# Kernel tuning notes

Hardware: AMD Instinct MI355X
Metric: run time of the kernel (lower is better)

The kernel has to match this reference:

```python
import jax, jax.numpy as jnp
import numpy as np

DIM = 1024
HEADS = 16
HEAD_DIM = DIM // HEADS
EPS = 1e-5


def _layer_norm(z, g, b):
    m = jnp.mean(z, axis=-1, keepdims=True)
    v = jnp.var(z, axis=-1, keepdims=True)
    return (z - m) * jax.lax.rsqrt(v + EPS) * g + b


def setup_inputs() -> dict:
    key = jax.random.key(0)
    ks = jax.random.split(key, 8)
    B, T, S = 2, 2048, 2048
    x = jax.random.normal(ks[0], (B, T, DIM), dtype=jnp.float32)
    context = jax.random.normal(ks[1], (B, S, DIM), dtype=jnp.float32)
    w_qkv = jax.random.normal(ks[2], (DIM, 3 * DIM), dtype=jnp.float32) * 0.02
    b_qkv = jnp.zeros((3 * DIM,), dtype=jnp.float32)
    w_out = jax.random.normal(ks[3], (DIM, DIM), dtype=jnp.float32) * 0.02
    b_out = jnp.zeros((DIM,), dtype=jnp.float32)
    ln_g = jnp.ones((DIM,), dtype=jnp.float32)
    ln_b = jnp.zeros((DIM,), dtype=jnp.float32)
    return {"x": x, "context": context, "w_qkv": w_qkv, "b_qkv": b_qkv,
            "w_out": w_out, "b_out": b_out, "ln_g": ln_g, "ln_b": ln_b}


def reference(x, context, w_qkv, b_qkv, w_out, b_out, ln_g, ln_b):
    B, T, C = x.shape
    S = context.shape[1]
    scale = HEAD_DIM ** -0.5

    def split_heads(z):  # [B, L, C] -> [B, H, L, Dh]
        return z.reshape(z.shape[0], z.shape[1], HEADS, HEAD_DIM).transpose(0, 2, 1, 3)

    # self qkv
    qkv = _layer_norm(x, ln_g, ln_b) @ w_qkv + b_qkv  # [B, T, 3C]
    q = split_heads(qkv[..., :C])
    k = split_heads(qkv[..., C:2 * C])
    v = split_heads(qkv[..., 2 * C:])

    # context k, v from the shared qkv projection (K/V slices)
    ckv = _layer_norm(context, ln_g, ln_b) @ w_qkv + b_qkv  # [B, S, 3C]
    ck = split_heads(ckv[..., C:2 * C])
    cv = split_heads(ckv[..., 2 * C:])

    k = jnp.concatenate([k, ck], axis=2)  # [B, H, T+S, Dh]
    v = jnp.concatenate([v, cv], axis=2)

    attn = jax.nn.softmax(jnp.einsum('bhtd,bhsd->bhts', q, k) * scale, axis=-1)
    out = jnp.einsum('bhts,bhsd->bhtd', attn, v)  # [B, H, T, Dh]
    out = out.transpose(0, 2, 1, 3).reshape(B, T, C)
    return out @ w_out + b_out + x
```

## Files before the change

kernel.cpp:

```cpp
#include <hip/hip_runtime.h>
#include <stdint.h>

#define H 16
#define DH 64
#define T 2048
#define SS 2048
#define L 4096
#define DIM 1024
#define BB 2

typedef __bf16 bf16x8 __attribute__((ext_vector_type(8)));
typedef float f32x4 __attribute__((ext_vector_type(4)));
typedef float f32x16 __attribute__((ext_vector_type(16)));
typedef unsigned u32x4 __attribute__((ext_vector_type(4)));

__device__ __forceinline__ unsigned short f2bf(float f){
  unsigned u = __builtin_bit_cast(unsigned, f);
  u += 0x7fff + ((u >> 16) & 1);
  return (unsigned short)(u >> 16);
}

__device__ __forceinline__ unsigned cvt_pk_bf16(float lo, float hi){
  unsigned r;
  asm("v_cvt_pk_bf16_f32 %0, %1, %2" : "=v"(r) : "v"(lo), "v"(hi));
  return r;
}

__device__ __forceinline__ float fmax3(float a, float b, float c){
  float r;
  asm("v_max3_f32 %0, %1, %2, %3" : "=v"(r) : "v"(a), "v"(b), "v"(c));
  return r;
}

__device__ __forceinline__ void gload_lds16(const void* g, void* l){
  void* gnc = const_cast<void*>(g);
  __builtin_amdgcn_global_load_lds((__attribute__((address_space(1))) void*)gnc,
                                   (__attribute__((address_space(3))) void*)l, 16, 0, 0);
}

__global__ __launch_bounds__(256) void ln_kernel(const float* __restrict__ x, const float* __restrict__ ctx,
                          const float* __restrict__ g, const float* __restrict__ b,
                          unsigned short* __restrict__ out){
  int row = blockIdx.x;
  int tid = threadIdx.x;
  const float* src = (row < BB*T) ? (x + (size_t)row*DIM) : (ctx + (size_t)(row - BB*T)*DIM);
  float4 v = reinterpret_cast<const float4*>(src)[tid];
  float s  = v.x + v.y + v.z + v.w;
  float s2 = v.x*v.x + v.y*v.y + v.z*v.z + v.w*v.w;
  #pragma unroll
  for (int off = 32; off > 0; off >>= 1){
    s  += __shfl_down(s,  off, 64);
    s2 += __shfl_down(s2, off, 64);
  }
  __shared__ float red[8];
  if ((tid & 63) == 0){ red[(tid>>6)*2] = s; red[(tid>>6)*2+1] = s2; }
  __syncthreads();
  s  = red[0] + red[2] + red[4] + red[6];
  s2 = red[1] + red[3] + red[5] + red[7];
  float mean = s * (1.0f/DIM);
  float var  = s2 * (1.0f/DIM) - mean*mean;
  float rstd = rsqrtf(var + 1e-5f);
  float4 gg = reinterpret_cast<const float4*>(g)[tid];
  float4 bv = reinterpret_cast<const float4*>(b)[tid];
  ushort4 o;
  o.x = f2bf((v.x-mean)*rstd*gg.x + bv.x);
  o.y = f2bf((v.y-mean)*rstd*gg.y + bv.y);
  o.z = f2bf((v.z-mean)*rstd*gg.z + bv.z);
  o.w = f2bf((v.w-mean)*rstd*gg.w + bv.w);
  reinterpret_cast<ushort4*>(out + (size_t)row*DIM)[tid] = o;
}

__global__ __launch_bounds__(256) void transpose_f32_bf16(const float* __restrict__ in,
                          unsigned short* __restrict__ out, int R, int C){
  __shared__ float tile[32][33];
  int c0 = blockIdx.x*32, r0 = blockIdx.y*32;
  int tx = threadIdx.x & 31, ty = threadIdx.x >> 5;
  #pragma unroll
  for (int k = 0; k < 4; k++)
    tile[ty + k*8][tx] = in[(size_t)(r0 + ty + k*8)*C + c0 + tx];
  __syncthreads();
  #pragma unroll
  for (int k = 0; k < 4; k++)
    out[(size_t)(c0 + ty + k*8)*R + r0 + tx] = f2bf(tile[tx][ty + k*8]);
}

__global__ __launch_bounds__(256) void qkv_gemm(const unsigned short* __restrict__ A,
      const unsigned short* __restrict__ Bt, const float* __restrict__ bias,
      unsigned short* __restrict__ qbuf, unsigned short* __restrict__ kbuf,
      unsigned short* __restrict__ vtbuf){
  int orig = blockIdx.x;
  int xcd = orig & 7, wid = orig >> 3;
  int mblk = ((wid & 7) << 3) + xcd;
  int nblk = wid >> 3;
  int n0 = nblk*128, m0 = mblk*128;
  if (m0 >= BB*T && n0 < DIM) return;
  __shared__ union {
    struct { unsigned short at[2][128*32]; unsigned short bt[2][128*32]; } s;
    unsigned short ct[128][136];
    unsigned short vt[128][136];
  } u;
  int tid = threadIdx.x, lane = tid & 63, wv = tid >> 6;
  int wm = (wv >> 1)*64, wn = (wv & 1)*64;
  f32x4 acc[4][4];
  #pragma unroll
  for (int i = 0; i < 4; i++)
    #pragma unroll
    for (int j = 0; j < 4; j++) acc[i][j] = (f32x4){0.f,0.f,0.f,0.f};

  #define QSTAGE(bufi, k0) { \
    _Pragma("unroll") \
    for (int c = 0; c < 2; c++){ \
      int idx = c*256 + tid; \
      int row = idx >> 2, koff = (idx & 3)*16; \
      gload_lds16((const char*)A  + ((size_t)(m0+row)*DIM + (k0))*2 + koff, \
                  (char*)u.s.at[bufi] + (c*256 + wv*64)*16); \
      gload_lds16((const char*)Bt + ((size_t)(n0+row)*DIM + (k0))*2 + koff, \
                  (char*)u.s.bt[bufi] + (c*256 + wv*64)*16); \
    } }

  QSTAGE(0, 0);
  __syncthreads();

  for (int kt = 0; kt < 32; kt++){
    int bufi = kt & 1;
    if (kt + 1 < 32) QSTAGE(bufi^1, (kt+1)*32);
    bf16x8 af[4], bfv[4];
    #pragma unroll
    for (int i = 0; i < 4; i++){
      af[i]  = *reinterpret_cast<const bf16x8*>((const char*)u.s.at[bufi] + (wm + i*16 + (lane&15))*64 + (lane>>4)*16);
      bfv[i] = *reinterpret_cast<const bf16x8*>((const char*)u.s.bt[bufi] + (wn + i*16 + (lane&15))*64 + (lane>>4)*16);
    }
    #pragma unroll
    for (int mi = 0; mi < 4; mi++)
      #pragma unroll
      for (int ni = 0; ni < 4; ni++)
        acc[mi][ni] = __builtin_amdgcn_mfma_f32_16x16x32_bf16(af[mi], bfv[ni], acc[mi][ni], 0,0,0);
    __syncthreads();
  }

  int sec = n0 >> 10;
  if (sec < 2){
    float scale = (sec == 0) ? 0.18033688f : 1.0f;
    #pragma unroll
    for (int ni = 0; ni < 4; ni++){
      int nl = wn + ni*16 + (lane & 15);
      float bv = bias[n0 + nl];
      #pragma unroll
      for (int mi = 0; mi < 4; mi++){
        int ml = wm + mi*16 + ((lane >> 4) << 2);
        #pragma unroll
        for (int r = 0; r < 4; r++)
          u.ct[ml + r][nl] = f2bf((acc[mi][ni][r] + bv)*scale);
      }
    }
    __syncthreads();
    #pragma unroll
    for (int c = 0; c < 8; c++){
      int idx = c*256 + tid;
      int row = idx >> 4, ch = idx & 15;
      bf16x8 v = *reinterpret_cast<const bf16x8*>(&u.ct[row][ch*8]);
      int gm = m0 + row, gn = n0 + ch*8;
      int cc = gn & 1023, hh2 = cc >> 6, d = cc & 63;
      bool isctx = gm >= BB*T;
      int rm = isctx ? gm - BB*T : gm;
      int bidx = rm >> 11, tt = rm & 2047;
      size_t bh2 = (size_t)bidx*H + hh2;
      if (sec == 0){
        *reinterpret_cast<bf16x8*>(qbuf + (bh2*T + tt)*DH + d) = v;
      } else {
        int j = isctx ? T + tt : tt;
        *reinterpret_cast<bf16x8*>(kbuf + (bh2*L + j)*DH + d) = v;
      }
    }
  } else {
    #pragma unroll
    for (int ni = 0; ni < 4; ni++){
      int nl = wn + ni*16 + (lane & 15);
      float bv = bias[n0 + nl];
      #pragma unroll
      for (int mi = 0; mi < 4; mi++){
        int ml = wm + mi*16 + ((lane >> 4) << 2);
        ushort4 o;
        o.x = f2bf(acc[mi][ni][0] + bv);
        o.y = f2bf(acc[mi][ni][1] + bv);
        o.z = f2bf(acc[mi][ni][2] + bv);
        o.w = f2bf(acc[mi][ni][3] + bv);
        *reinterpret_cast<ushort4*>(&u.vt[nl][ml]) = o;
      }
    }
    __syncthreads();
    #pragma unroll
    for (int c = 0; c < 8; c++){
      int idx = c*256 + tid;
      int nl = idx >> 4, ch = idx & 15;
      bf16x8 v = *reinterpret_cast<const bf16x8*>(&u.vt[nl][ch*8]);
      int gn = n0 + nl;
      int cc = gn & 1023, hh2 = cc >> 6, d = cc & 63;
      int gm = m0 + ch*8;
      bool isctx = gm >= BB*T;
      int rm = isctx ? gm - BB*T : gm;
      int bidx = rm >> 11, tt = rm & 2047;
      int j = isctx ? T + tt : tt;
      size_t bh2 = (size_t)bidx*H + hh2;
      *reinterpret_cast<bf16x8*>(vtbuf + (bh2*DH + d)*L + j) = v;
    }
  }
}

__global__ __launch_bounds__(256, 4) void attn_kernel(const unsigned short* __restrict__ q,
      const unsigned short* __restrict__ kbuf, const unsigned short* __restrict__ vtbuf,
      unsigned short* __restrict__ obuf, float* __restrict__ mbuf, float* __restrict__ lbuf){
  int hw = blockIdx.x;
  int wid = (hw & 7)*128 + (hw >> 3);
  int qt = wid & 15, bh = (wid >> 4) & 31, cb = wid >> 9;
  int hh = bh & 15, b = bh >> 4;
  int tid = threadIdx.x, lane = tid & 63, wv = tid >> 6;
  int hi = lane >> 5, q32 = lane & 31;
  __shared__ unsigned short kt[2][64*64];
  __shared__ unsigned short vtt[2][64*64];
  size_t bhs = (size_t)b*H + hh;
  int qbase = qt*128 + wv*32;

  const unsigned short* qp = q + (bhs*T + qbase + q32)*DH + hi*8;
  bf16x8 qf[4];
  #pragma unroll
  for (int ks = 0; ks < 4; ks++)
    qf[ks] = *reinterpret_cast<const bf16x8*>(qp + ks*16);

  bf16x8 ones;
  #pragma unroll
  for (int j = 0; j < 8; j++) ones[j] = (__bf16)1.0f;

  f32x16 o_acc[2], l_vec;
  #pragma unroll
  for (int d = 0; d < 2; d++)
    #pragma unroll
    for (int i = 0; i < 16; i++) o_acc[d][i] = 0.f;
  #pragma unroll
  for (int i = 0; i < 16; i++) l_vec[i] = 0.f;
  float m_l = -1e30f;

  const char* kg = (const char*)(kbuf + bhs*(size_t)L*DH) + (size_t)cb*2048*128;
  const char* vg = (const char*)(vtbuf + bhs*(size_t)DH*L) + (size_t)cb*4096;

  #define STAGE(bufi, jt) { \
    _Pragma("unroll") \
    for (int c = 0; c < 2; c++){ \
      int idx = c*256 + tid; \
      int row = idx >> 3, c16 = idx & 7; \
      int sc16 = c16 ^ (row & 7); \
      gload_lds16(kg + (size_t)((jt)*64 + row)*128 + sc16*16, \
                  (char*)kt[bufi] + (c*256 + wv*64)*16); \
      gload_lds16(vg + (size_t)row*(L*2) + (jt)*128 + sc16*16, \
                  (char*)vtt[bufi] + (c*256 + wv*64)*16); \
    } }

  STAGE(0, 0);
  __syncthreads();

  for (int jt = 0; jt < 32; ++jt){
    int bufi = jt & 1;
    if (jt + 1 < 32) STAGE(bufi^1, jt+1);
    const char* kb = (const char*)kt[bufi];
    const char* vb = (const char*)vtt[bufi];

    f32x16 sc[2];
    #pragma unroll
    for (int t = 0; t < 2; t++)
      #pragma unroll
      for (int i = 0; i < 16; i++) sc[t][i] = 0.f;
    #pragma unroll
    for (int ks = 0; ks < 4; ks++){
      #pragma unroll
      for (int t = 0; t < 2; t++){
        int row = t*32 + q32;
        bf16x8 kf = *reinterpret_cast<const bf16x8*>(kb + row*128 + (((ks*2+hi) ^ (row&7))*16));
        sc[t] = __builtin_amdgcn_mfma_f32_32x32x16_bf16(kf, qf[ks], sc[t], 0,0,0);
      }
    }

    float rt[2];
    #pragma unroll
    for (int t = 0; t < 2; t++){
      float v0 = fmax3(sc[t][0],  sc[t][1],  sc[t][2]);
      float v1 = fmax3(sc[t][3],  sc[t][4],  sc[t][5]);
      float v2 = fmax3(sc[t][6],  sc[t][7],  sc[t][8]);
      float v3 = fmax3(sc[t][9],  sc[t][10], sc[t][11]);
      float v4 = fmax3(sc[t][12], sc[t][13], sc[t][14]);
      rt[t] = fmaxf(fmax3(v0, v1, v2), fmax3(v3, v4, sc[t][15]));
    }
    float tm = fmaxf(rt[0], rt[1]);

    if (!__all(tm - m_l <= 8.0f)){
      float tmf = fmaxf(tm, __shfl_xor(tm, 32, 64));
      float mn = fmaxf(m_l, tmf);
      float alpha = __builtin_amdgcn_exp2f(m_l - mn);
      m_l = mn;
      #pragma unroll
      for (int d = 0; d < 2; d++)
        #pragma unroll
        for (int i = 0; i < 16; i++) o_acc[d][i] *= alpha;
      l_vec[0] *= alpha;
    }
    #pragma unroll
    for (int t = 0; t < 2; t++)
      #pragma unroll
      for (int i = 0; i < 16; i++)
        sc[t][i] = __builtin_amdgcn_exp2f(sc[t][i] - m_l);

    bf16x8 pfrag[4];
    #pragma unroll
    for (int t = 0; t < 2; t++){
      #pragma unroll
      for (int half = 0; half < 2; half++){
        unsigned p01 = cvt_pk_bf16(sc[t][half*8+0], sc[t][half*8+1]);
        unsigned p23 = cvt_pk_bf16(sc[t][half*8+2], sc[t][half*8+3]);
        unsigned p45 = cvt_pk_bf16(sc[t][half*8+4], sc[t][half*8+5]);
        unsigned p67 = cvt_pk_bf16(sc[t][half*8+6], sc[t][half*8+7]);
        asm("v_permlane32_swap_b32 %0, %1" : "+v"(p01), "+v"(p45));
        asm("v_permlane32_swap_b32 %0, %1" : "+v"(p23), "+v"(p67));
        u32x4 w = (u32x4){p01, p23, p45, p67};
        pfrag[t*2 + half] = __builtin_bit_cast(bf16x8, w);
      }
    }

    #pragma unroll
    for (int ks = 0; ks < 4; ks++){
      #pragma unroll
      for (int d = 0; d < 2; d++){
        int row = d*32 + q32;
        bf16x8 vf = *reinterpret_cast<const bf16x8*>(vb + row*128 + (((ks*2+hi) ^ (row&7))*16));
        o_acc[d] = __builtin_amdgcn_mfma_f32_32x32x16_bf16(vf, pfrag[ks], o_acc[d], 0,0,0);
      }
      l_vec = __builtin_amdgcn_mfma_f32_32x32x16_bf16(ones, pfrag[ks], l_vec, 0,0,0);
    }
    __syncthreads();
  }

  float inv = 1.0f / l_vec[0];
  unsigned short* aop = obuf + (size_t)cb*BB*H*T*DH + ((size_t)bh*T + qbase + q32)*DH;
  #pragma unroll
  for (int d = 0; d < 2; d++)
    #pragma unroll
    for (int rg = 0; rg < 4; rg++){
      int d0 = d*32 + rg*8 + hi*4;
      ushort4 o;
      o.x = __builtin_bit_cast(unsigned short, (__bf16)(o_acc[d][rg*4+0]*inv));
      o.y = __builtin_bit_cast(unsigned short, (__bf16)(o_acc[d][rg*4+1]*inv));
      o.z = __builtin_bit_cast(unsigned short, (__bf16)(o_acc[d][rg*4+2]*inv));
      o.w = __builtin_bit_cast(unsigned short, (__bf16)(o_acc[d][rg*4+3]*inv));
      *reinterpret_cast<ushort4*>(aop + d0) = o;
    }
  if (hi == 0){
    size_t mi = ((size_t)cb*BB*H + bh)*T + qbase + q32;
    mbuf[mi] = m_l;
    lbuf[mi] = l_vec[0];
  }
}

__global__ __launch_bounds__(256) void attn_combine(const unsigned short* __restrict__ obuf,
      const float* __restrict__ mbuf, const float* __restrict__ lbuf,
      unsigned short* __restrict__ ao){
  int gid = blockIdx.x*256 + threadIdx.x;
  int d8 = gid & 7;
  int qg = gid >> 3;
  int qq = qg & (T-1);
  int bh = qg >> 11;
  int b = bh >> 4, h = bh & 15;
  float m0 = mbuf[(size_t)qg];
  float m1 = mbuf[(size_t)BB*H*T + qg];
  float l0 = lbuf[(size_t)qg];
  float l1 = lbuf[(size_t)BB*H*T + qg];
  float mm = fmaxf(m0, m1);
  float w0 = l0 * __builtin_amdgcn_exp2f(m0 - mm);
  float w1 = l1 * __builtin_amdgcn_exp2f(m1 - mm);
  float inv = 1.0f / (w0 + w1);
  w0 *= inv; w1 *= inv;
  bf16x8 o0 = *reinterpret_cast<const bf16x8*>(obuf + (size_t)qg*DH + d8*8);
  bf16x8 o1 = *reinterpret_cast<const bf16x8*>(obuf + (size_t)BB*H*T*DH + (size_t)qg*DH + d8*8);
  bf16x8 res;
  #pragma unroll
  for (int j = 0; j < 8; j++)
    res[j] = (__bf16)(w0*(float)o0[j] + w1*(float)o1[j]);
  *reinterpret_cast<bf16x8*>(ao + ((size_t)b*T + qq)*DIM + h*DH + d8*8) = res;
}

__global__ __launch_bounds__(256) void out_gemm(const unsigned short* __restrict__ A,
      const unsigned short* __restrict__ Bt, const float* __restrict__ bout,
      const float* __restrict__ xres, float* __restrict__ out){
  int n0 = blockIdx.x*128, m0 = blockIdx.y*128;
  __shared__ unsigned short at[2][128*32];
  __shared__ unsigned short btile[2][128*32];
  int tid = threadIdx.x, lane = tid & 63, wv = tid >> 6;
  int wm = (wv >> 1)*64, wn = (wv & 1)*64;
  f32x4 acc[4][4];
  #pragma unroll
  for (int i = 0; i < 4; i++)
    #pragma unroll
    for (int j = 0; j < 4; j++) acc[i][j] = (f32x4){0.f,0.f,0.f,0.f};

  #define OSTAGE(bufi, k0) { \
    _Pragma("unroll") \
    for (int c = 0; c < 2; c++){ \
      int idx = c*256 + tid; \
      int row = idx >> 2, koff = (idx & 3)*16; \
      gload_lds16((const char*)A  + ((size_t)(m0+row)*DIM + (k0))*2 + koff, \
                  (char*)at[bufi] + (c*256 + wv*64)*16); \
      gload_lds16((const char*)Bt + ((size_t)(n0+row)*DIM + (k0))*2 + koff, \
                  (char*)btile[bufi] + (c*256 + wv*64)*16); \
    } }

  OSTAGE(0, 0);
  __syncthreads();

  for (int kt = 0; kt < 32; kt++){
    int bufi = kt & 1;
    if (kt + 1 < 32) OSTAGE(bufi^1, (kt+1)*32);
    bf16x8 af[4], bfv[4];
    #pragma unroll
    for (int i = 0; i < 4; i++){
      af[i]  = *reinterpret_cast<const bf16x8*>((const char*)at[bufi]    + (wm + i*16 + (lane&15))*64 + (lane>>4)*16);
      bfv[i] = *reinterpret_cast<const bf16x8*>((const char*)btile[bufi] + (wn + i*16 + (lane&15))*64 + (lane>>4)*16);
    }
    #pragma unroll
    for (int mi = 0; mi < 4; mi++)
      #pragma unroll
      for (int ni = 0; ni < 4; ni++)
        acc[mi][ni] = __builtin_amdgcn_mfma_f32_16x16x32_bf16(af[mi], bfv[ni], acc[mi][ni], 0,0,0);
    __syncthreads();
  }

  #pragma unroll
  for (int ni = 0; ni < 4; ni++){
    int gn = n0 + wn + ni*16 + (lane & 15);
    float bv = bout[gn];
    #pragma unroll
    for (int mi = 0; mi < 4; mi++){
      int gmb = m0 + wm + mi*16 + ((lane >> 4) << 2);
      #pragma unroll
      for (int r = 0; r < 4; r++){
        int gm = gmb + r;
        out[(size_t)gm*DIM + gn] = acc[mi][ni][r] + bv + xres[(size_t)gm*DIM + gn];
      }
    }
  }
}

extern "C" void kernel_launch(void* const* d_in, const int* in_sizes, int n_in,
                              void* d_out, int out_size, void* d_ws, size_t ws_size,
                              hipStream_t stream){
  const float* x    = (const float*)d_in[0];
  const float* ctx  = (const float*)d_in[1];
  const float* wqkv = (const float*)d_in[2];
  const float* bqkv = (const float*)d_in[3];
  const float* wout = (const float*)d_in[4];
  const float* bout = (const float*)d_in[5];
  const float* lng  = (const float*)d_in[6];
  const float* lnb  = (const float*)d_in[7];
  float* out = (float*)d_out;

  char* ws = (char*)d_ws;
  unsigned short* wqkvT  = (unsigned short*)ws; ws += (size_t)3072*1024*2;
  unsigned short* woutT  = (unsigned short*)ws; ws += (size_t)1024*1024*2;
  unsigned short* ln_all = (unsigned short*)ws; ws += (size_t)8192*1024*2;
  unsigned short* qbuf   = (unsigned short*)ws; ws += (size_t)BB*H*T*DH*2;
  unsigned short* kbuf   = (unsigned short*)ws; ws += (size_t)BB*H*L*DH*2;
  unsigned short* vtbuf  = (unsigned short*)ws; ws += (size_t)BB*H*DH*L*2;
  unsigned short* aobuf  = (unsigned short*)ws; ws += (size_t)BB*T*DIM*2;

  unsigned short* obuf = ln_all;
  float* mbuf = (float*)wqkvT;
  float* lbuf = mbuf + (size_t)2*BB*H*T;

  transpose_f32_bf16<<<dim3(3072/32, 1024/32), dim3(256), 0, stream>>>(wqkv, wqkvT, 1024, 3072);
  transpose_f32_bf16<<<dim3(1024/32, 1024/32), dim3(256), 0, stream>>>(wout, woutT, 1024, 1024);
  ln_kernel<<<dim3(8192), dim3(256), 0, stream>>>(x, ctx, lng, lnb, ln_all);
  qkv_gemm<<<dim3(1536), dim3(256), 0, stream>>>(ln_all, wqkvT, bqkv, qbuf, kbuf, vtbuf);
  attn_kernel<<<dim3(1024), dim3(256), 0, stream>>>(qbuf, kbuf, vtbuf, obuf, mbuf, lbuf);
  attn_combine<<<dim3(BB*H*T*8/256), dim3(256), 0, stream>>>(obuf, mbuf, lbuf, aobuf);
  out_gemm<<<dim3(1024/128, 4096/128), dim3(256), 0, stream>>>(aobuf, woutT, bout, x, out);
}
```

Before: 213.7 us.

## Use persistent atomic tile scheduler for QKV GEMM and halve out GEMM M-tile

The QKV GEMM becomes a persistent kernel. 1024 blocks pull tile indices from a global atomic counter, which a new tiny kernel zeroes first, and the tile-index remapping skips the Q tiles of context rows. The old launch of 1536 blocks had many blocks that exited at once. The output GEMM switches to 64x128 tiles to double its block count and improve wave fill across CUs. The cost is an extra launch, atomic serialization per tile, and lower arithmetic intensity in the output GEMM.

```diff
diff --git a/kernel.cpp b/kernel.cpp
--- a/kernel.cpp
+++ b/kernel.cpp
@@ -84,126 +84,139 @@
     out[(size_t)(c0 + ty + k*8)*R + r0 + tx] = f2bf(tile[tx][ty + k*8]);
 }
 
+__global__ __launch_bounds__(64) void zero_ctr(unsigned* __restrict__ c){
+  if (threadIdx.x == 0) *c = 0u;
+}
+
 __global__ __launch_bounds__(256) void qkv_gemm(const unsigned short* __restrict__ A,
       const unsigned short* __restrict__ Bt, const float* __restrict__ bias,
       unsigned short* __restrict__ qbuf, unsigned short* __restrict__ kbuf,
-      unsigned short* __restrict__ vtbuf){
-  int orig = blockIdx.x;
-  int xcd = orig & 7, wid = orig >> 3;
-  int mblk = ((wid & 7) << 3) + xcd;
-  int nblk = wid >> 3;
-  int n0 = nblk*128, m0 = mblk*128;
-  if (m0 >= BB*T && n0 < DIM) return;
+      unsigned short* __restrict__ vtbuf, unsigned* __restrict__ ctr){
   __shared__ union {
     struct { unsigned short at[2][128*32]; unsigned short bt[2][128*32]; } s;
     unsigned short ct[128][136];
     unsigned short vt[128][136];
   } u;
+  __shared__ unsigned s_g;
   int tid = threadIdx.x, lane = tid & 63, wv = tid >> 6;
   int wm = (wv >> 1)*64, wn = (wv & 1)*64;
-  f32x4 acc[4][4];
-  #pragma unroll
-  for (int i = 0; i < 4; i++)
-    #pragma unroll
-    for (int j = 0; j < 4; j++) acc[i][j] = (f32x4){0.f,0.f,0.f,0.f};
-
-  #define QSTAGE(bufi, k0) { \
-    _Pragma("unroll") \
-    for (int c = 0; c < 2; c++){ \
-      int idx = c*256 + tid; \
-      int row = idx >> 2, koff = (idx & 3)*16; \
-      gload_lds16((const char*)A  + ((size_t)(m0+row)*DIM + (k0))*2 + koff, \
-                  (char*)u.s.at[bufi] + (c*256 + wv*64)*16); \
-      gload_lds16((const char*)Bt + ((size_t)(n0+row)*DIM + (k0))*2 + koff, \
-                  (char*)u.s.bt[bufi] + (c*256 + wv*64)*16); \
-    } }
-
-  QSTAGE(0, 0);
-  __syncthreads();
-
-  for (int kt = 0; kt < 32; kt++){
-    int bufi = kt & 1;
-    if (kt + 1 < 32) QSTAGE(bufi^1, (kt+1)*32);
-    bf16x8 af[4], bfv[4];
-    #pragma unroll
-    for (int i = 0; i < 4; i++){
-      af[i]  = *reinterpret_cast<const bf16x8*>((const char*)u.s.at[bufi] + (wm + i*16 + (lane&15))*64 + (lane>>4)*16);
-      bfv[i] = *reinterpret_cast<const bf16x8*>((const char*)u.s.bt[bufi] + (wn + i*16 + (lane&15))*64 + (lane>>4)*16);
-    }
-    #pragma unroll
-    for (int mi = 0; mi < 4; mi++)
-      #pragma unroll
-      for (int ni = 0; ni < 4; ni++)
-        acc[mi][ni] = __builtin_amdgcn_mfma_f32_16x16x32_bf16(af[mi], bfv[ni], acc[mi][ni], 0,0,0);
+
+  for (;;){
+    if (tid == 0) s_g = atomicAdd(ctr, 1u);
     __syncthreads();
-  }
-
-  int sec = n0 >> 10;
-  if (sec < 2){
-    float scale = (sec == 0) ? 0.18033688f : 1.0f;
-    #pragma unroll
-    for (int ni = 0; ni < 4; ni++){
-      int nl = wn + ni*16 + (lane & 15);
-      float bv = bias[n0 + nl];
-      #pragma unroll
-      for (int mi = 0; mi < 4; mi++){
-        int ml = wm + mi*16 + ((lane >> 4) << 2);
+    unsigned g = s_g;
+    if (g >= 1280u) return;
+    int xcd = g & 7, a = g >> 3;
+    int w = (a < 32) ? ((a >> 2)*8 + (a & 3)) : (a + 32);
+    int mblk = ((w & 7) << 3) + xcd;
+    int nblk = w >> 3;
+    int n0 = nblk*128, m0 = mblk*128;
+
+    f32x4 acc[4][4];
+    #pragma unroll
+    for (int i = 0; i < 4; i++)
+      #pragma unroll
+      for (int j = 0; j < 4; j++) acc[i][j] = (f32x4){0.f,0.f,0.f,0.f};
+
+    #define QSTAGE(bufi, k0) { \
+      _Pragma("unroll") \
+      for (int c = 0; c < 2; c++){ \
+        int idx = c*256 + tid; \
+        int row = idx >> 2, koff = (idx & 3)*16; \
+        gload_lds16((const char*)A  + ((size_t)(m0+row)*DIM + (k0))*2 + koff, \
+                    (char*)u.s.at[bufi] + (c*256 + wv*64)*16); \
+        gload_lds16((const char*)Bt + ((size_t)(n0+row)*DIM + (k0))*2 + koff, \
+                    (char*)u.s.bt[bufi] + (c*256 + wv*64)*16); \
+      } }
+
+    QSTAGE(0, 0);
+    __syncthreads();
+
+    for (int kt = 0; kt < 32; kt++){
+      int bufi = kt & 1;
+      if (kt + 1 < 32) QSTAGE(bufi^1, (kt+1)*32);
+      bf16x8 af[4], bfv[4];
+      #pragma unroll
+      for (int i = 0; i < 4; i++){
+        af[i]  = *reinterpret_cast<const bf16x8*>((const char*)u.s.at[bufi] + (wm + i*16 + (lane&15))*64 + (lane>>4)*16);
+        bfv[i] = *reinterpret_cast<const bf16x8*>((const char*)u.s.bt[bufi] + (wn + i*16 + (lane&15))*64 + (lane>>4)*16);
+      }
+      #pragma unroll
+      for (int mi = 0; mi < 4; mi++)
         #pragma unroll
-        for (int r = 0; r < 4; r++)
-          u.ct[ml + r][nl] = f2bf((acc[mi][ni][r] + bv)*scale);
+        for (int ni = 0; ni < 4; ni++)
+          acc[mi][ni] = __builtin_amdgcn_mfma_f32_16x16x32_bf16(af[mi], bfv[ni], acc[mi][ni], 0,0,0);
+      __syncthreads();
+    }
+
+    int sec = n0 >> 10;
+    if (sec < 2){
+      float scale = (sec == 0) ? 0.18033688f : 1.0f;
+      #pragma unroll
+      for (int ni = 0; ni < 4; ni++){
+        int nl = wn + ni*16 + (lane & 15);
+        float bv = bias[n0 + nl];
+        #pragma unroll
+        for (int mi = 0; mi < 4; mi++){
+          int ml = wm + mi*16 + ((lane >> 4) << 2);
+          #pragma unroll
+          for (int r = 0; r < 4; r++)
+            u.ct[ml + r][nl] = f2bf((acc[mi][ni][r] + bv)*scale);
+        }
+      }
+      __syncthreads();
+      #pragma unroll
+      for (int c = 0; c < 8; c++){
+        int idx = c*256 + tid;
+        int row = idx >> 4, ch = idx & 15;
+        bf16x8 v = *reinterpret_cast<const bf16x8*>(&u.ct[row][ch*8]);
+        int gm = m0 + row, gn = n0 + ch*8;
+        int cc = gn & 1023, hh2 = cc >> 6, d = cc & 63;
+        bool isctx = gm >= BB*T;
+        int rm = isctx ? gm - BB*T : gm;
+        int bidx = rm >> 11, tt = rm & 2047;
+        size_t bh2 = (size_t)bidx*H + hh2;
+        if (sec == 0){
+          *reinterpret_cast<bf16x8*>(qbuf + (bh2*T + tt)*DH + d) = v;
+        } else {
+          int j = isctx ? T + tt : tt;
+          *reinterpret_cast<bf16x8*>(kbuf + (bh2*L + j)*DH + d) = v;
+        }
+      }
+    } else {
+      #pragma unroll
+      for (int ni = 0; ni < 4; ni++){
+        int nl = wn + ni*16 + (lane & 15);
+        float bv = bias[n0 + nl];
+        #pragma unroll
+        for (int mi = 0; mi < 4; mi++){
+          int ml = wm + mi*16 + ((lane >> 4) << 2);
+          ushort4 o;
+          o.x = f2bf(acc[mi][ni][0] + bv);
+          o.y = f2bf(acc[mi][ni][1] + bv);
+          o.z = f2bf(acc[mi][ni][2] + bv);
+          o.w = f2bf(acc[mi][ni][3] + bv);
+          *reinterpret_cast<ushort4*>(&u.vt[nl][ml]) = o;
+        }
+      }
+      __syncthreads();
+      #pragma unroll
+      for (int c = 0; c < 8; c++){
+        int idx = c*256 + tid;
+        int nl = idx >> 4, ch = idx & 15;
+        bf16x8 v = *reinterpret_cast<const bf16x8*>(&u.vt[nl][ch*8]);
+        int gn = n0 + nl;
+        int cc = gn & 1023, hh2 = cc >> 6, d = cc & 63;
+        int gm = m0 + ch*8;
+        bool isctx = gm >= BB*T;
+        int rm = isctx ? gm - BB*T : gm;
+        int bidx = rm >> 11, tt = rm & 2047;
+        int j = isctx ? T + tt : tt;
+        size_t bh2 = (size_t)bidx*H + hh2;
+        *reinterpret_cast<bf16x8*>(vtbuf + (bh2*DH + d)*L + j) = v;
       }
     }
     __syncthreads();
-    #pragma unroll
-    for (int c = 0; c < 8; c++){
-      int idx = c*256 + tid;
-      int row = idx >> 4, ch = idx & 15;
-      bf16x8 v = *reinterpret_cast<const bf16x8*>(&u.ct[row][ch*8]);
-      int gm = m0 + row, gn = n0 + ch*8;
-      int cc = gn & 1023, hh2 = cc >> 6, d = cc & 63;
-      bool isctx = gm >= BB*T;
-      int rm = isctx ? gm - BB*T : gm;
-      int bidx = rm >> 11, tt = rm & 2047;
-      size_t bh2 = (size_t)bidx*H + hh2;
-      if (sec == 0){
-        *reinterpret_cast<bf16x8*>(qbuf + (bh2*T + tt)*DH + d) = v;
-      } else {
-        int j = isctx ? T + tt : tt;
-        *reinterpret_cast<bf16x8*>(kbuf + (bh2*L + j)*DH + d) = v;
-      }
-    }
-  } else {
-    #pragma unroll
-    for (int ni = 0; ni < 4; ni++){
-      int nl = wn + ni*16 + (lane & 15);
-      float bv = bias[n0 + nl];
-      #pragma unroll
-      for (int mi = 0; mi < 4; mi++){
-        int ml = wm + mi*16 + ((lane >> 4) << 2);
-        ushort4 o;
-        o.x = f2bf(acc[mi][ni][0] + bv);
-        o.y = f2bf(acc[mi][ni][1] + bv);
-        o.z = f2bf(acc[mi][ni][2] + bv);
-        o.w = f2bf(acc[mi][ni][3] + bv);
-        *reinterpret_cast<ushort4*>(&u.vt[nl][ml]) = o;
-      }
-    }
-    __syncthreads();
-    #pragma unroll
-    for (int c = 0; c < 8; c++){
-      int idx = c*256 + tid;
-      int nl = idx >> 4, ch = idx & 15;
-      bf16x8 v = *reinterpret_cast<const bf16x8*>(&u.vt[nl][ch*8]);
-      int gn = n0 + nl;
-      int cc = gn & 1023, hh2 = cc >> 6, d = cc & 63;
-      int gm = m0 + ch*8;
-      bool isctx = gm >= BB*T;
-      int rm = isctx ? gm - BB*T : gm;
-      int bidx = rm >> 11, tt = rm & 2047;
-      int j = isctx ? T + tt : tt;
-      size_t bh2 = (size_t)bidx*H + hh2;
-      *reinterpret_cast<bf16x8*>(vtbuf + (bh2*DH + d)*L + j) = v;
-    }
   }
 }
 
@@ -388,24 +401,25 @@
 __global__ __launch_bounds__(256) void out_gemm(const unsigned short* __restrict__ A,
       const unsigned short* __restrict__ Bt, const float* __restrict__ bout,
       const float* __restrict__ xres, float* __restrict__ out){
-  int n0 = blockIdx.x*128, m0 = blockIdx.y*128;
-  __shared__ unsigned short at[2][128*32];
+  int n0 = blockIdx.x*128, m0 = blockIdx.y*64;
+  __shared__ unsigned short at[2][64*32];
   __shared__ unsigned short btile[2][128*32];
   int tid = threadIdx.x, lane = tid & 63, wv = tid >> 6;
-  int wm = (wv >> 1)*64, wn = (wv & 1)*64;
-  f32x4 acc[4][4];
-  #pragma unroll
-  for (int i = 0; i < 4; i++)
+  int wm = (wv >> 1)*32, wn = (wv & 1)*64;
+  f32x4 acc[2][4];
+  #pragma unroll
+  for (int i = 0; i < 2; i++)
     #pragma unroll
     for (int j = 0; j < 4; j++) acc[i][j] = (f32x4){0.f,0.f,0.f,0.f};
 
   #define OSTAGE(bufi, k0) { \
+    { int row = tid >> 2, koff = (tid & 3)*16; \
+      gload_lds16((const char*)A + ((size_t)(m0+row)*DIM + (k0))*2 + koff, \
+                  (char*)at[bufi] + (wv*64)*16); } \
     _Pragma("unroll") \
     for (int c = 0; c < 2; c++){ \
       int idx = c*256 + tid; \
       int row = idx >> 2, koff = (idx & 3)*16; \
-      gload_lds16((const char*)A  + ((size_t)(m0+row)*DIM + (k0))*2 + koff, \
-                  (char*)at[bufi] + (c*256 + wv*64)*16); \
       gload_lds16((const char*)Bt + ((size_t)(n0+row)*DIM + (k0))*2 + koff, \
                   (char*)btile[bufi] + (c*256 + wv*64)*16); \
     } }
@@ -416,14 +430,15 @@
   for (int kt = 0; kt < 32; kt++){
     int bufi = kt & 1;
     if (kt + 1 < 32) OSTAGE(bufi^1, (kt+1)*32);
-    bf16x8 af[4], bfv[4];
-    #pragma unroll
-    for (int i = 0; i < 4; i++){
-      af[i]  = *reinterpret_cast<const bf16x8*>((const char*)at[bufi]    + (wm + i*16 + (lane&15))*64 + (lane>>4)*16);
+    bf16x8 af[2], bfv[4];
+    #pragma unroll
+    for (int i = 0; i < 2; i++)
+      af[i]  = *reinterpret_cast<const bf16x8*>((const char*)at[bufi] + (wm + i*16 + (lane&15))*64 + (lane>>4)*16);
+    #pragma unroll
+    for (int i = 0; i < 4; i++)
       bfv[i] = *reinterpret_cast<const bf16x8*>((const char*)btile[bufi] + (wn + i*16 + (lane&15))*64 + (lane>>4)*16);
-    }
-    #pragma unroll
-    for (int mi = 0; mi < 4; mi++)
+    #pragma unroll
+    for (int mi = 0; mi < 2; mi++)
       #pragma unroll
       for (int ni = 0; ni < 4; ni++)
         acc[mi][ni] = __builtin_amdgcn_mfma_f32_16x16x32_bf16(af[mi], bfv[ni], acc[mi][ni], 0,0,0);
@@ -435,7 +450,7 @@
     int gn = n0 + wn + ni*16 + (lane & 15);
     float bv = bout[gn];
     #pragma unroll
-    for (int mi = 0; mi < 4; mi++){
+    for (int mi = 0; mi < 2; mi++){
       int gmb = m0 + wm + mi*16 + ((lane >> 4) << 2);
       #pragma unroll
       for (int r = 0; r < 4; r++){
@@ -471,12 +486,14 @@
   unsigned short* obuf = ln_all;
   float* mbuf = (float*)wqkvT;
   float* lbuf = mbuf + (size_t)2*BB*H*T;
+  unsigned* qctr = (unsigned*)aobuf;
 
   transpose_f32_bf16<<<dim3(3072/32, 1024/32), dim3(256), 0, stream>>>(wqkv, wqkvT, 1024, 3072);
   transpose_f32_bf16<<<dim3(1024/32, 1024/32), dim3(256), 0, stream>>>(wout, woutT, 1024, 1024);
   ln_kernel<<<dim3(8192), dim3(256), 0, stream>>>(x, ctx, lng, lnb, ln_all);
-  qkv_gemm<<<dim3(1536), dim3(256), 0, stream>>>(ln_all, wqkvT, bqkv, qbuf, kbuf, vtbuf);
+  zero_ctr<<<dim3(1), dim3(64), 0, stream>>>(qctr);
+  qkv_gemm<<<dim3(1024), dim3(256), 0, stream>>>(ln_all, wqkvT, bqkv, qbuf, kbuf, vtbuf, qctr);
   attn_kernel<<<dim3(1024), dim3(256), 0, stream>>>(qbuf, kbuf, vtbuf, obuf, mbuf, lbuf);
   attn_combine<<<dim3(BB*H*T*8/256), dim3(256), 0, stream>>>(obuf, mbuf, lbuf, aobuf);
-  out_gemm<<<dim3(1024/128, 4096/128), dim3(256), 0, stream>>>(aobuf, woutT, bout, x, out);
-}
+  out_gemm<<<dim3(1024/128, 4096/64), dim3(256), 0, stream>>>(aobuf, woutT, bout, x, out);
+}
```

Result: slower. 240.8 us (+12.7%).
